# Performance work log

Measured on AMD Instinct MI355X. Metric: run time of the kernel, lower is better.

Reference implementation:

```python
import jax, jax.numpy as jnp
import numpy as np

N_LAYERS = 6
N_HEADS = 16
HIDDEN = 1024
HEAD = HIDDEN // N_HEADS  # 64
FFWD = 4096
VOCAB = 32000
WIN = 512
EMBED = 128
BATCH = 4
NEG_INF = -1.0e9


def layer_norm(x, bias, scale, eps=1e-6):
    m = jnp.mean(x, axis=-1, keepdims=True)
    v = jnp.mean(jnp.square(x - m), axis=-1, keepdims=True)
    return (x - m) * jax.lax.rsqrt(v + eps) * scale + bias


def setup_inputs() -> dict:
    key = jax.random.key(0)
    ks = jax.random.split(key, 16)

    def rn(k, shape):
        return 0.1 * jax.random.normal(k, shape, jnp.float32)

    return {
        "x_input": jax.random.randint(ks[0], (BATCH, WIN), 0, VOCAB),
        "prev_inputs": jax.random.normal(ks[1], (N_LAYERS, BATCH, WIN, HIDDEN), jnp.float32),
        "W_emb_dec": rn(ks[2], (VOCAB, EMBED)),
        "W_dec_lin": rn(ks[3], (EMBED, HIDDEN)),
        "p_decoder": rn(ks[4], (HIDDEN, VOCAB)),
        "p_d_q": rn(ks[5], (N_LAYERS, HIDDEN, HIDDEN)),
        "p_d_k": rn(ks[6], (N_LAYERS, HIDDEN, HIDDEN)),
        "p_d_v": rn(ks[7], (N_LAYERS, HIDDEN, HIDDEN)),
        "p_d_c": rn(ks[8], (N_LAYERS, HIDDEN, HIDDEN)),
        "p_d_ff1": rn(ks[9], (N_LAYERS, HIDDEN, FFWD)),
        "p_d_ff2": rn(ks[10], (N_LAYERS, FFWD, HIDDEN)),
        "b_d_ff1": jnp.zeros((N_LAYERS, FFWD), jnp.float32),
        "b_d_ff2": jnp.zeros((N_LAYERS, HIDDEN), jnp.float32),
        "b_d_bias_1": jnp.zeros((N_LAYERS, HIDDEN), jnp.float32),
        "b_d_bias_2": jnp.zeros((N_LAYERS, HIDDEN), jnp.float32),
        "b_d_scale_1": jnp.ones((N_LAYERS, HIDDEN), jnp.float32),
        "b_d_scale_2": jnp.ones((N_LAYERS, HIDDEN), jnp.float32),
        "x_emb_pos_dec": rn(ks[11], (N_LAYERS, 2 * WIN, HIDDEN)),
    }


def reference(x_input, prev_inputs, W_emb_dec, W_dec_lin, p_decoder,
              p_d_q, p_d_k, p_d_v, p_d_c, p_d_ff1, p_d_ff2,
              b_d_ff1, b_d_ff2, b_d_bias_1, b_d_bias_2,
              b_d_scale_1, b_d_scale_2, x_emb_pos_dec):
    L = x_input.shape[1]
    # token embedding (scaled by 1/sqrt(hidden)) then linear to hidden
    tok = W_emb_dec[x_input] * (HIDDEN ** -0.5)        # [B, L, E]
    h0 = jnp.einsum('ble,eh->blh', tok, W_dec_lin)     # [B, L, H]

    mask_len = L + WIN
    mask = NEG_INF * (1.0 - jnp.tril(jnp.ones((mask_len, mask_len), jnp.float32)))

    def split_heads(x):
        b, t, _ = x.shape
        return x.reshape(b, t, N_HEADS, HEAD).transpose(0, 2, 1, 3)  # [B, nH, T, d]

    def layer_fn(layer_input, p):
        Wq, Wk, Wv, Wc, Wf1, Wf2, bf1, bf2, b1, s1, b2, s2, pos, prev = p
        # concat cached window with current input, add positional embedding
        x = pos[None] + jnp.concatenate([prev, layer_input], axis=1)  # [B, 2W, H]
        q = split_heads(x @ Wq) * (HEAD ** -0.5)
        k = split_heads(x @ Wk)
        v = split_heads(x @ Wv)
        scores = jnp.einsum('bhqd,bhkd->bhqk', q, k) + mask
        alphas = jax.nn.softmax(scores, axis=-1)
        o = jnp.einsum('bhqk,bhkd->bhqd', alphas, v)
        o = o.transpose(0, 2, 1, 3).reshape(x.shape)  # combine heads
        attn = o @ Wc
        # var_type == 'norm_add': residual + LN(sublayer)
        x_self = x + layer_norm(attn, b1, s1)
        ff = jnp.maximum(x_self @ Wf1 + bf1, 0.0) @ Wf2 + bf2
        y = x_self + layer_norm(ff, b2, s2)
        new = y[:, WIN:, :]  # drop the cached-window positions
        return new, new

    params = (p_d_q, p_d_k, p_d_v, p_d_c, p_d_ff1, p_d_ff2,
              b_d_ff1, b_d_ff2, b_d_bias_1, b_d_scale_1,
              b_d_bias_2, b_d_scale_2, x_emb_pos_dec, prev_inputs)
    _, dec_outputs = jax.lax.scan(layer_fn, h0, params)  # [n_layers, B, L, H]
    dec_logits = jnp.einsum('blh,hv->blv', dec_outputs[-1], p_decoder)
    return (dec_logits, dec_outputs)
```

## Files before the change

### kernel.cpp

```cpp
#include <hip/hip_runtime.h>
#include <hip/hip_bf16.h>

#define NL   6
#define NH   16
#define HID  1024
#define HD   64
#define FFW  4096
#define VOC  32000
#define WINN 512
#define EMB  128
#define NB   4
#define TT   1024

typedef __attribute__((ext_vector_type(8))) _Float16 f16x8;
typedef __attribute__((ext_vector_type(8))) short    b16x8;
typedef __attribute__((ext_vector_type(4))) float    f32x4;

__device__ __forceinline__ ushort f2b(float f) {
    __hip_bfloat16 h = __float2bfloat16(f);
    return *reinterpret_cast<ushort*>(&h);
}
__device__ __forceinline__ void split16(float f, ushort& hb, ushort& lb) {
    _Float16 h = (_Float16)f;
    _Float16 l = (_Float16)((f - (float)h) * 2048.0f);
    hb = __builtin_bit_cast(ushort, h);
    lb = __builtin_bit_cast(ushort, l);
}
__device__ __forceinline__ void gload16(const void* g, void* l) {
    __builtin_amdgcn_global_load_lds(
        (const __attribute__((address_space(1))) unsigned int*)g,
        (__attribute__((address_space(3))) unsigned int*)l, 16, 0, 0);
}

__global__ __launch_bounds__(256) void embed_kernel(
    const int* __restrict__ xin, const float* __restrict__ Wemb,
    const float* __restrict__ Wlin, float* __restrict__ h0)
{
    int row = blockIdx.x;
    int tok = xin[row];
    __shared__ float tk[EMB];
    if (threadIdx.x < EMB) tk[threadIdx.x] = Wemb[tok * EMB + threadIdx.x] * 0.03125f;
    __syncthreads();
    for (int j = 0; j < 4; ++j) {
        int c = threadIdx.x + 256 * j;
        float acc = 0.f;
        for (int e = 0; e < EMB; ++e) acc += tk[e] * Wlin[e * HID + c];
        h0[(long)row * HID + c] = acc;
    }
}

__global__ __launch_bounds__(256) void build_x_kernel(
    const float* __restrict__ pos, const float* __restrict__ prev,
    const float* __restrict__ cur, float* __restrict__ x,
    ushort* __restrict__ xh, ushort* __restrict__ xl)
{
    int i4 = blockIdx.x * blockDim.x + threadIdx.x;
    if (i4 >= NB * TT * HID / 4) return;
    int h4 = i4 % (HID / 4);
    int bt = i4 / (HID / 4);
    int t = bt % TT, b = bt / TT;
    float4 p = ((const float4*)pos)[t * (HID / 4) + h4];
    float4 s;
    if (t < WINN) s = ((const float4*)prev)[(long)(b * WINN + t) * (HID / 4) + h4];
    else          s = ((const float4*)cur)[(long)(b * WINN + (t - WINN)) * (HID / 4) + h4];
    float4 r; r.x = p.x + s.x; r.y = p.y + s.y; r.z = p.z + s.z; r.w = p.w + s.w;
    ((float4*)x)[i4] = r;
    ushort4 uh, ul;
    split16(r.x, uh.x, ul.x); split16(r.y, uh.y, ul.y);
    split16(r.z, uh.z, ul.z); split16(r.w, uh.w, ul.w);
    ((ushort4*)xh)[i4] = uh;
    ((ushort4*)xl)[i4] = ul;
}

__global__ __launch_bounds__(256) void wsplit_kernel(
    const float* __restrict__ W, ushort* __restrict__ Wth, ushort* __restrict__ Wtl,
    int K, int N)
{
    __shared__ float ts[32][33];
    int n0 = blockIdx.x * 32, k0 = blockIdx.y * 32;
    int tr = threadIdx.x >> 5, tc = threadIdx.x & 31;
#pragma unroll
    for (int j = 0; j < 4; ++j)
        ts[tr + j * 8][tc] = W[(long)(k0 + tr + j * 8) * N + n0 + tc];
    __syncthreads();
#pragma unroll
    for (int j = 0; j < 4; ++j) {
        int n = tr + j * 8;
        ushort hb, lb;
        split16(ts[tc][n], hb, lb);
        long idx = (long)(n0 + n) * K + k0 + tc;
        Wth[idx] = hb;
        Wtl[idx] = lb;
    }
}

__global__ __launch_bounds__(256) void vtrans_kernel(
    const ushort* __restrict__ vh, const ushort* __restrict__ vl,
    ushort* __restrict__ vth, ushort* __restrict__ vtl, int src_stride)
{
    __shared__ ushort th[32][33], tl[32][33];
    int n0 = blockIdx.x * 32, r0 = blockIdx.y * 32;
    int tr = threadIdx.x >> 5, tc = threadIdx.x & 31;
#pragma unroll
    for (int j = 0; j < 4; ++j) {
        long g = (long)(r0 + tr + j * 8) * src_stride + n0 + tc;
        th[tr + j * 8][tc] = vh[g];
        tl[tr + j * 8][tc] = vl[g];
    }
    __syncthreads();
#pragma unroll
    for (int j = 0; j < 4; ++j) {
        long g = (long)(n0 + tr + j * 8) * (NB * TT) + r0 + tc;
        vth[g] = th[tc][tr + j * 8];
        vtl[g] = tl[tc][tr + j * 8];
    }
}

__global__ __launch_bounds__(256) void hgemm(
    const ushort* __restrict__ Ah, const ushort* __restrict__ Al,
    const ushort* __restrict__ Bh, const ushort* __restrict__ Bl,
    float* __restrict__ Cf0, float* __restrict__ Cf1,
    int M, int N, int K_stride, int Ksub,
    float scale, const float* __restrict__ bias, int relu, int amap)
{
    __shared__ __align__(16) ushort Ash[128 * 32];
    __shared__ __align__(16) ushort Asl[128 * 32];
    __shared__ __align__(16) ushort Bsh[64 * 32];
    __shared__ __align__(16) ushort Bsl[64 * 32];
    const int tid  = threadIdx.x;
    const int rb   = blockIdx.y * 128;
    const int cb   = blockIdx.x * 64;
    const int z    = blockIdx.z;
    const int k_off = z * Ksub;
    float* __restrict__ Cf = z ? Cf1 : Cf0;
    const float* bias_eff = (z == 0) ? bias : nullptr;
    const int wave = tid >> 6, lane = tid & 63;
    const int wr   = (wave >> 1) * 64;
    const int wc   = (wave & 1) * 32;
    const int lr   = lane & 15;
    const int kh   = lane >> 4;

    const int lrow = lane >> 2;
    const int lkc  = (lane & 3) * 8;
    int ga0 = rb + wave * 32 + lrow;
    int ga1 = ga0 + 16;
    long ma0 = amap ? (long)((ga0 >> 9) * 1024 + 512 + (ga0 & 511)) : (long)ga0;
    long ma1 = amap ? (long)((ga1 >> 9) * 1024 + 512 + (ga1 & 511)) : (long)ga1;
    const ushort* gAh0 = Ah + ma0 * K_stride + k_off + lkc;
    const ushort* gAh1 = Ah + ma1 * K_stride + k_off + lkc;
    const ushort* gAl0 = Al + ma0 * K_stride + k_off + lkc;
    const ushort* gAl1 = Al + ma1 * K_stride + k_off + lkc;
    const ushort* gBh0 = Bh + (long)(cb + wave * 16 + lrow) * K_stride + k_off + lkc;
    const ushort* gBl0 = Bl + (long)(cb + wave * 16 + lrow) * K_stride + k_off + lkc;
    ushort* lAh0 = Ash + wave * 1024;
    ushort* lAh1 = Ash + wave * 1024 + 512;
    ushort* lAl0 = Asl + wave * 1024;
    ushort* lAl1 = Asl + wave * 1024 + 512;
    ushort* lBh0 = Bsh + wave * 512;
    ushort* lBl0 = Bsl + wave * 512;

    int aoff[4], boff[2];
#pragma unroll
    for (int m = 0; m < 4; ++m) aoff[m] = (wr + m * 16 + lr) * 32 + kh * 8;
#pragma unroll
    for (int n = 0; n < 2; ++n) boff[n] = (wc + n * 16 + lr) * 32 + kh * 8;

    f32x4 accH[4][2], accL[4][2];
#pragma unroll
    for (int m = 0; m < 4; ++m)
#pragma unroll
        for (int n = 0; n < 2; ++n) {
            accH[m][n] = (f32x4){0.f, 0.f, 0.f, 0.f};
            accL[m][n] = (f32x4){0.f, 0.f, 0.f, 0.f};
        }

    for (int k0 = 0; k0 < Ksub; k0 += 32) {
        __syncthreads();
        gload16(gAh0 + k0, lAh0);
        gload16(gAh1 + k0, lAh1);
        gload16(gAl0 + k0, lAl0);
        gload16(gAl1 + k0, lAl1);
        gload16(gBh0 + k0, lBh0);
        gload16(gBl0 + k0, lBl0);
        __syncthreads();
        f16x8 afh[4], afl[4], bfh[2], bfl[2];
#pragma unroll
        for (int m = 0; m < 4; ++m) {
            afh[m] = *(const f16x8*)(Ash + aoff[m]);
            afl[m] = *(const f16x8*)(Asl + aoff[m]);
        }
#pragma unroll
        for (int n = 0; n < 2; ++n) {
            bfh[n] = *(const f16x8*)(Bsh + boff[n]);
            bfl[n] = *(const f16x8*)(Bsl + boff[n]);
        }
#pragma unroll
        for (int m = 0; m < 4; ++m)
#pragma unroll
            for (int n = 0; n < 2; ++n) {
                accH[m][n] = __builtin_amdgcn_mfma_f32_16x16x32_f16(afh[m], bfh[n], accH[m][n], 0, 0, 0);
                accL[m][n] = __builtin_amdgcn_mfma_f32_16x16x32_f16(afh[m], bfl[n], accL[m][n], 0, 0, 0);
                accL[m][n] = __builtin_amdgcn_mfma_f32_16x16x32_f16(afl[m], bfh[n], accL[m][n], 0, 0, 0);
            }
    }

#pragma unroll
    for (int m = 0; m < 4; ++m) {
        int row0 = rb + wr + m * 16 + kh * 4;
#pragma unroll
        for (int n = 0; n < 2; ++n) {
            int col = cb + wc + n * 16 + lr;
            float bv = bias_eff ? bias_eff[col] : 0.f;
#pragma unroll
            for (int r = 0; r < 4; ++r) {
                float v = (accH[m][n][r] + accL[m][n][r] * (1.f / 2048.f)) * scale + bv;
                if (relu) v = fmaxf(v, 0.f);
                Cf[(long)(row0 + r) * N + col] = v;
            }
        }
    }
}

__global__ __launch_bounds__(512) void hgemm8(
    const ushort* __restrict__ Ah, const ushort* __restrict__ Al,
    const ushort* __restrict__ Bh, const ushort* __restrict__ Bl,
    ushort* __restrict__ Chh, ushort* __restrict__ Cll,
    int M, int N, int K_stride,
    float scale, const float* __restrict__ bias, int relu)
{
    __shared__ __align__(16) ushort Ash[128 * 32];
    __shared__ __align__(16) ushort Asl[128 * 32];
    __shared__ __align__(16) ushort Bsh[128 * 32];
    __shared__ __align__(16) ushort Bsl[128 * 32];
    const int tid  = threadIdx.x;
    const int rb   = blockIdx.y * 128;
    const int cb   = blockIdx.x * 128;
    const int wave = tid >> 6, lane = tid & 63;
    const int wr   = (wave >> 2) * 64;
    const int wc   = (wave & 3) * 32;
    const int lr   = lane & 15;
    const int kh   = lane >> 4;

    const int lrow = lane >> 2;
    const int lkc  = (lane & 3) * 8;
    const ushort* gA_h = Ah + (long)(rb + wave * 16 + lrow) * K_stride + lkc;
    const ushort* gA_l = Al + (long)(rb + wave * 16 + lrow) * K_stride + lkc;
    const ushort* gB_h = Bh + (long)(cb + wave * 16 + lrow) * K_stride + lkc;
    const ushort* gB_l = Bl + (long)(cb + wave * 16 + lrow) * K_stride + lkc;
    ushort* lA_h = Ash + wave * 512;
    ushort* lA_l = Asl + wave * 512;
    ushort* lB_h = Bsh + wave * 512;
    ushort* lB_l = Bsl + wave * 512;

    int aoff[4], boff[2];
#pragma unroll
    for (int m = 0; m < 4; ++m) aoff[m] = (wr + m * 16 + lr) * 32 + kh * 8;
#pragma unroll
    for (int n = 0; n < 2; ++n) boff[n] = (wc + n * 16 + lr) * 32 + kh * 8;

    f32x4 accH[4][2], accL[4][2];
#pragma unroll
    for (int m = 0; m < 4; ++m)
#pragma unroll
        for (int n = 0; n < 2; ++n) {
            accH[m][n] = (f32x4){0.f, 0.f, 0.f, 0.f};
            accL[m][n] = (f32x4){0.f, 0.f, 0.f, 0.f};
        }

    for (int k0 = 0; k0 < K_stride; k0 += 32) {
        __syncthreads();
        gload16(gA_h + k0, lA_h);
        gload16(gA_l + k0, lA_l);
        gload16(gB_h + k0, lB_h);
        gload16(gB_l + k0, lB_l);
        __syncthreads();
        f16x8 afh[4], afl[4], bfh[2], bfl[2];
#pragma unroll
        for (int m = 0; m < 4; ++m) {
            afh[m] = *(const f16x8*)(Ash + aoff[m]);
            afl[m] = *(const f16x8*)(Asl + aoff[m]);
        }
#pragma unroll
        for (int n = 0; n < 2; ++n) {
            bfh[n] = *(const f16x8*)(Bsh + boff[n]);
            bfl[n] = *(const f16x8*)(Bsl + boff[n]);
        }
#pragma unroll
        for (int m = 0; m < 4; ++m)
#pragma unroll
            for (int n = 0; n < 2; ++n) {
                accH[m][n] = __builtin_amdgcn_mfma_f32_16x16x32_f16(afh[m], bfh[n], accH[m][n], 0, 0, 0);
                accL[m][n] = __builtin_amdgcn_mfma_f32_16x16x32_f16(afh[m], bfl[n], accL[m][n], 0, 0, 0);
                accL[m][n] = __builtin_amdgcn_mfma_f32_16x16x32_f16(afl[m], bfh[n], accL[m][n], 0, 0, 0);
            }
    }

#pragma unroll
    for (int m = 0; m < 4; ++m) {
        int row0 = rb + wr + m * 16 + kh * 4;
#pragma unroll
        for (int n = 0; n < 2; ++n) {
            int col = cb + wc + n * 16 + lr;
            float bv = bias ? bias[col] : 0.f;
#pragma unroll
            for (int r = 0; r < 4; ++r) {
                float v = (accH[m][n][r] + accL[m][n][r] * (1.f / 2048.f)) * scale + bv;
                if (relu) v = fmaxf(v, 0.f);
                long idx = (long)(row0 + r) * N + col;
                ushort hb, lb; split16(v, hb, lb);
                Chh[idx] = hb; Cll[idx] = lb;
            }
        }
    }
}

__global__ __launch_bounds__(256) void fattn_mfma(
    const float* __restrict__ qa, const float* __restrict__ qb,
    const ushort* __restrict__ kbh, const ushort* __restrict__ kbl, int kstr,
    const ushort* __restrict__ vth, const ushort* __restrict__ vtl,
    ushort* __restrict__ oh, ushort* __restrict__ ol)
{
    __shared__ __align__(16) ushort ksh[64 * 72];
    __shared__ __align__(16) ushort ksl[64 * 72];
    __shared__ __align__(16) ushort vsh[64 * 72];
    __shared__ __align__(16) ushort vsl[64 * 72];
    const int qt = blockIdx.x, h = blockIdx.y, b = blockIdx.z;
    const int tid = threadIdx.x;
    const int wave = tid >> 6, lane = tid & 63;
    const int lr = lane & 15, kg4 = lane >> 4;
    const int qbase = b * WINN + qt * 64;

    f16x8 qfh[2], qfl[2];
#pragma unroll
    for (int c = 0; c < 2; ++c) {
        long ga = (long)(qbase + wave * 16 + lr) * HID + h * HD + c * 32 + kg4 * 8;
        float4 a0 = *(const float4*)(qa + ga);
        float4 a1 = *(const float4*)(qa + ga + 4);
        float4 b0 = *(const float4*)(qb + ga);
        float4 b1 = *(const float4*)(qb + ga + 4);
        float qv[8] = {a0.x + b0.x, a0.y + b0.y, a0.z + b0.z, a0.w + b0.w,
                       a1.x + b1.x, a1.y + b1.y, a1.z + b1.z, a1.w + b1.w};
        ushort uh[8], ul[8];
#pragma unroll
        for (int j = 0; j < 8; ++j) split16(qv[j], uh[j], ul[j]);
        qfh[c] = *(const f16x8*)uh;
        qfl[c] = *(const f16x8*)ul;
    }

    f32x4 accOH[4], accOL[4];
#pragma unroll
    for (int d = 0; d < 4; ++d) {
        accOH[d] = (f32x4){0.f, 0.f, 0.f, 0.f};
        accOL[d] = (f32x4){0.f, 0.f, 0.f, 0.f};
    }
    float mrow[4], lrow[4];
#pragma unroll
    for (int r = 0; r < 4; ++r) { mrow[r] = -3.0e38f; lrow[r] = 0.f; }

    const int sr = tid >> 2;
    const int sd = (tid & 3) * 16;

    const int ktmax = 9 + qt;
    for (int kt = 0; kt < ktmax; ++kt) {
        __syncthreads();
        {
            long gk = (long)(b * TT + kt * 64 + sr) * kstr + h * HD + sd;
            uint4 h0 = *(const uint4*)(kbh + gk);
            uint4 h1 = *(const uint4*)(kbh + gk + 8);
            uint4 l0 = *(const uint4*)(kbl + gk);
            uint4 l1 = *(const uint4*)(kbl + gk + 8);
            long gv = (long)(h * HD + sr) * (NB * TT) + b * TT + kt * 64 + sd;
            uint4 vh0 = *(const uint4*)(vth + gv);
            uint4 vh1 = *(const uint4*)(vth + gv + 8);
            uint4 vl0 = *(const uint4*)(vtl + gv);
            uint4 vl1 = *(const uint4*)(vtl + gv + 8);
            *(uint4*)(ksh + sr * 72 + sd) = h0;
            *(uint4*)(ksh + sr * 72 + sd + 8) = h1;
            *(uint4*)(ksl + sr * 72 + sd) = l0;
            *(uint4*)(ksl + sr * 72 + sd + 8) = l1;
            *(uint4*)(vsh + sr * 72 + sd) = vh0;
            *(uint4*)(vsh + sr * 72 + sd + 8) = vh1;
            *(uint4*)(vsl + sr * 72 + sd) = vl0;
            *(uint4*)(vsl + sr * 72 + sd + 8) = vl1;
        }
        __syncthreads();

        f32x4 sH[4], sL[4];
#pragma unroll
        for (int n = 0; n < 4; ++n) {
            sH[n] = (f32x4){0.f, 0.f, 0.f, 0.f};
            sL[n] = (f32x4){0.f, 0.f, 0.f, 0.f};
        }
#pragma unroll
        for (int c = 0; c < 2; ++c) {
#pragma unroll
            for (int n = 0; n < 4; ++n) {
                int ad = (n * 16 + lr) * 72 + c * 32 + kg4 * 8;
                f16x8 bh = *(const f16x8*)(ksh + ad);
                f16x8 bl = *(const f16x8*)(ksl + ad);
                sH[n] = __builtin_amdgcn_mfma_f32_16x16x32_f16(qfh[c], bh, sH[n], 0, 0, 0);
                sL[n] = __builtin_amdgcn_mfma_f32_16x16x32_f16(qfh[c], bl, sL[n], 0, 0, 0);
                sL[n] = __builtin_amdgcn_mfma_f32_16x16x32_f16(qfl[c], bh, sL[n], 0, 0, 0);
            }
        }
        float S[4][4];
#pragma unroll
        for (int n = 0; n < 4; ++n)
#pragma unroll
            for (int r = 0; r < 4; ++r)
                S[n][r] = sH[n][r] + sL[n][r] * (1.f / 2048.f);

        if (kt == ktmax - 1) {
#pragma unroll
            for (int r = 0; r < 4; ++r) {
                int qi = WINN + qt * 64 + wave * 16 + kg4 * 4 + r;
#pragma unroll
                for (int n = 0; n < 4; ++n) {
                    int kg = kt * 64 + n * 16 + lr;
                    if (kg > qi) S[n][r] = -1e9f;
                }
            }
        }

#pragma unroll
        for (int r = 0; r < 4; ++r) {
            float mx = fmaxf(fmaxf(S[0][r], S[1][r]), fmaxf(S[2][r], S[3][r]));
            mx = fmaxf(mx, __shfl_xor(mx, 1));
            mx = fmaxf(mx, __shfl_xor(mx, 2));
            mx = fmaxf(mx, __shfl_xor(mx, 4));
            mx = fmaxf(mx, __shfl_xor(mx, 8));
            float mnew = fmaxf(mrow[r], mx);
            float alpha = __expf(mrow[r] - mnew);
            float rs = 0.f;
#pragma unroll
            for (int n = 0; n < 4; ++n) { S[n][r] = __expf(S[n][r] - mnew); rs += S[n][r]; }
            rs += __shfl_xor(rs, 1);
            rs += __shfl_xor(rs, 2);
            rs += __shfl_xor(rs, 4);
            rs += __shfl_xor(rs, 8);
            lrow[r] = lrow[r] * alpha + rs;
            mrow[r] = mnew;
#pragma unroll
            for (int d = 0; d < 4; ++d) { accOH[d][r] *= alpha; accOL[d][r] *= alpha; }
        }

        __syncthreads();
#pragma unroll
        for (int n = 0; n < 4; ++n)
#pragma unroll
            for (int r = 0; r < 4; ++r) {
                ushort hb, lb;
                split16(S[n][r], hb, lb);
                int ad = (wave * 16 + kg4 * 4 + r) * 72 + n * 16 + lr;
                ksh[ad] = hb;
                ksl[ad] = lb;
            }
        f16x8 pfh[2], pfl[2];
#pragma unroll
        for (int c = 0; c < 2; ++c) {
            int ad = (wave * 16 + lr) * 72 + c * 32 + kg4 * 8;
            pfh[c] = *(const f16x8*)(ksh + ad);
            pfl[c] = *(const f16x8*)(ksl + ad);
        }
#pragma unroll
        for (int c = 0; c < 2; ++c) {
#pragma unroll
            for (int d = 0; d < 4; ++d) {
                int ad = (d * 16 + lr) * 72 + c * 32 + kg4 * 8;
                f16x8 vh = *(const f16x8*)(vsh + ad);
                f16x8 vl = *(const f16x8*)(vsl + ad);
                accOH[d] = __builtin_amdgcn_mfma_f32_16x16x32_f16(pfh[c], vh, accOH[d], 0, 0, 0);
                accOL[d] = __builtin_amdgcn_mfma_f32_16x16x32_f16(pfh[c], vl, accOL[d], 0, 0, 0);
                accOL[d] = __builtin_amdgcn_mfma_f32_16x16x32_f16(pfl[c], vh, accOL[d], 0, 0, 0);
            }
        }
    }

#pragma unroll
    for (int r = 0; r < 4; ++r) {
        float inv = 1.f / lrow[r];
        long rowb = (long)(qbase + wave * 16 + kg4 * 4 + r) * HID + h * HD + lr;
#pragma unroll
        for (int d = 0; d < 4; ++d) {
            float v = (accOH[d][r] + accOL[d][r] * (1.f / 2048.f)) * inv;
            ushort hb, lb;
            split16(v, hb, lb);
            oh[rowb + d * 16] = hb;
            ol[rowb + d * 16] = lb;
        }
    }
}

__global__ __launch_bounds__(256) void transp_kernel(
    const float* __restrict__ W, ushort* __restrict__ Wt, int K, int N)
{
    __shared__ float ts[32][33];
    int n0 = blockIdx.x * 32, k0 = blockIdx.y * 32;
    int tr = threadIdx.x >> 5, tc = threadIdx.x & 31;
#pragma unroll
    for (int j = 0; j < 4; ++j)
        ts[tr + j * 8][tc] = W[(long)(k0 + tr + j * 8) * N + n0 + tc];
    __syncthreads();
#pragma unroll
    for (int j = 0; j < 4; ++j) {
        int n = tr + j * 8;
        Wt[(long)(n0 + n) * K + k0 + tc] = f2b(ts[tc][n]);
    }
}

__global__ __launch_bounds__(256) void mfma_gemm(
    const ushort* __restrict__ A, const ushort* __restrict__ Bt,
    float* __restrict__ Cf, int M, int N, int K)
{
    __shared__ __align__(16) ushort As[128 * 32];
    __shared__ __align__(16) ushort Bs[128 * 32];
    const int tid  = threadIdx.x;
    const int ntm  = M >> 7;
    const int nbx  = gridDim.x;
    const int nwg  = nbx * gridDim.y;
    const int bid  = blockIdx.y * nbx + blockIdx.x;
    const int cpx  = nwg >> 3;
    const int swz  = (bid & 7) * cpx + (bid >> 3);
    const int rb   = (swz % ntm) * 128;
    const int cb   = (swz / ntm) * 128;
    const int wave = tid >> 6, lane = tid & 63;
    const int wr   = (wave >> 1) * 64;
    const int wc   = (wave & 1) * 64;
    const int lr   = lane & 15;
    const int kh   = lane >> 4;

    const int lrow = lane >> 2;
    const int lkc  = (lane & 3) * 8;
    const ushort* gA0 = A + (long)(rb + wave * 32 + lrow) * K + lkc;
    const ushort* gA1 = A + (long)(rb + wave * 32 + 16 + lrow) * K + lkc;
    const ushort* gB0 = Bt + (long)(cb + wave * 32 + lrow) * K + lkc;
    const ushort* gB1 = Bt + (long)(cb + wave * 32 + 16 + lrow) * K + lkc;
    ushort* lA0 = As + wave * 1024;
    ushort* lA1 = As + wave * 1024 + 512;
    ushort* lB0 = Bs + wave * 1024;
    ushort* lB1 = Bs + wave * 1024 + 512;

    int aoff[4], boff[4];
#pragma unroll
    for (int m = 0; m < 4; ++m) aoff[m] = (wr + m * 16 + lr) * 32 + kh * 8;
#pragma unroll
    for (int n = 0; n < 4; ++n) boff[n] = (wc + n * 16 + lr) * 32 + kh * 8;

    f32x4 acc[4][4];
#pragma unroll
    for (int m = 0; m < 4; ++m)
#pragma unroll
        for (int n = 0; n < 4; ++n)
            acc[m][n] = (f32x4){0.f, 0.f, 0.f, 0.f};

    for (int k0 = 0; k0 < K; k0 += 32) {
        __syncthreads();
        gload16(gA0 + k0, lA0);
        gload16(gA1 + k0, lA1);
        gload16(gB0 + k0, lB0);
        gload16(gB1 + k0, lB1);
        __syncthreads();
        b16x8 af[4], bfr[4];
#pragma unroll
        for (int m = 0; m < 4; ++m) af[m] = *(const b16x8*)(As + aoff[m]);
#pragma unroll
        for (int n = 0; n < 4; ++n) bfr[n] = *(const b16x8*)(Bs + boff[n]);
#pragma unroll
        for (int m = 0; m < 4; ++m)
#pragma unroll
            for (int n = 0; n < 4; ++n)
                acc[m][n] = __builtin_amdgcn_mfma_f32_16x16x32_bf16(af[m], bfr[n], acc[m][n], 0, 0, 0);
    }

#pragma unroll
    for (int m = 0; m < 4; ++m) {
        int row0 = rb + wr + m * 16 + kh * 4;
#pragma unroll
        for (int n = 0; n < 4; ++n) {
            int col = cb + wc + n * 16 + lr;
#pragma unroll
            for (int r = 0; r < 4; ++r)
                Cf[(long)(row0 + r) * N + col] = acc[m][n][r];
        }
    }
}

__global__ __launch_bounds__(256) void ln_res_kernel(
    const float* __restrict__ t, const float* __restrict__ t2,
    const float* __restrict__ res, float* __restrict__ out,
    ushort* __restrict__ outh, ushort* __restrict__ outl, ushort* __restrict__ outb,
    const float* __restrict__ bias, const float* __restrict__ scale, int res_map)
{
    int r = blockIdx.x;
    int tid = threadIdx.x;
    long rr = res_map ? (long)((r >> 9) * 1024 + 512 + (r & 511)) : (long)r;
    float4 v = ((const float4*)(t + (long)r * HID))[tid];
    if (t2) {
        float4 w = ((const float4*)(t2 + (long)r * HID))[tid];
        v.x += w.x; v.y += w.y; v.z += w.z; v.w += w.w;
    }
    __shared__ float red[4];
    float s = v.x + v.y + v.z + v.w;
    for (int off = 32; off > 0; off >>= 1) s += __shfl_xor(s, off);
    if ((tid & 63) == 0) red[tid >> 6] = s;
    __syncthreads();
    float mean = (red[0] + red[1] + red[2] + red[3]) * (1.f / HID);
    __syncthreads();
    float dx = v.x - mean, dy = v.y - mean, dz = v.z - mean, dw = v.w - mean;
    float qs = dx * dx + dy * dy + dz * dz + dw * dw;
    for (int off = 32; off > 0; off >>= 1) qs += __shfl_xor(qs, off);
    if ((tid & 63) == 0) red[tid >> 6] = qs;
    __syncthreads();
    float var = (red[0] + red[1] + red[2] + red[3]) * (1.f / HID);
    float rs = rsqrtf(var + 1e-6f);
    float4 rv = ((const float4*)(res + rr * HID))[tid];
    float4 sc4 = ((const float4*)scale)[tid];
    float4 b4  = ((const float4*)bias)[tid];
    float4 o4;
    o4.x = rv.x + dx * rs * sc4.x + b4.x;
    o4.y = rv.y + dy * rs * sc4.y + b4.y;
    o4.z = rv.z + dz * rs * sc4.z + b4.z;
    o4.w = rv.w + dw * rs * sc4.w + b4.w;
    ((float4*)(out + (long)r * HID))[tid] = o4;
    if (outh) {
        ushort4 uh, ul;
        split16(o4.x, uh.x, ul.x); split16(o4.y, uh.y, ul.y);
        split16(o4.z, uh.z, ul.z); split16(o4.w, uh.w, ul.w);
        ((ushort4*)(outh + (long)r * HID))[tid] = uh;
        ((ushort4*)(outl + (long)r * HID))[tid] = ul;
    }
    if (outb) {
        ushort4 u; u.x = f2b(o4.x); u.y = f2b(o4.y); u.z = f2b(o4.z); u.w = f2b(o4.w);
        ((ushort4*)(outb + (long)r * HID))[tid] = u;
    }
}

extern "C" void kernel_launch(void* const* d_in, const int* in_sizes, int n_in,
                              void* d_out, int out_size, void* d_ws, size_t ws_size,
                              hipStream_t stream)
{
    const int*   x_input = (const int*)  d_in[0];
    const float* prev    = (const float*)d_in[1];
    const float* Wemb    = (const float*)d_in[2];
    const float* Wlin    = (const float*)d_in[3];
    const float* pdec    = (const float*)d_in[4];
    const float* pq      = (const float*)d_in[5];
    const float* pk      = (const float*)d_in[6];
    const float* pv      = (const float*)d_in[7];
    const float* pc      = (const float*)d_in[8];
    const float* pf1     = (const float*)d_in[9];
    const float* pf2     = (const float*)d_in[10];
    const float* bf1     = (const float*)d_in[11];
    const float* bf2     = (const float*)d_in[12];
    const float* b1      = (const float*)d_in[13];
    const float* b2      = (const float*)d_in[14];
    const float* s1      = (const float*)d_in[15];
    const float* s2      = (const float*)d_in[16];
    const float* pos     = (const float*)d_in[17];

    float* outp   = (float*)d_out;
    float* logits = outp;
    float* dec    = outp + (long)2048 * VOC;

    char* base = (char*)d_ws;
    float*  x_f   = (float*) (base + 0);
    ushort* x_hi  = (ushort*)(base + 16777216);
    ushort* x_lo  = (ushort*)(base + 25165824);
    ushort* kv_hi = (ushort*)(base + 33554432);
    ushort* kv_lo = (ushort*)(base + 50331648);
    ushort* vt_hi = (ushort*)(base + 67108864);
    ushort* vt_lo = (ushort*)(base + 75497472);
    ushort* o_hi  = (ushort*)(base + 83886080);
    ushort* o_lo  = (ushort*)(base + 88080384);
    float*  t0a   = (float*) (base + 92274688);
    float*  h0    = t0a;
    float*  qa    = t0a;
    float*  t0b   = (float*) (base + 100663296);
    float*  qb    = t0b;
    float*  xs    = (float*) (base + 109051904);
    ushort* xs_hi = (ushort*)(base + 117440512);
    ushort* xs_lo = (ushort*)(base + 121634816);
    ushort* wq_hi = (ushort*)(base + 125829120);
    ushort* wq_lo = (ushort*)(base + 127926272);
    ushort* wkv_hi= (ushort*)(base + 130023424);
    ushort* wkv_lo= (ushort*)(base + 134217728);
    ushort* wc_hi = (ushort*)(base + 138412032);
    ushort* wc_lo = (ushort*)(base + 140509184);
    ushort* wf1_hi= (ushort*)(base + 142606336);
    ushort* wf1_lo= (ushort*)(base + 150994944);
    ushort* wf2_hi= (ushort*)(base + 159383552);
    ushort* wf2_lo= (ushort*)(base + 167772160);
    ushort* ff1_hi= (ushort*)(base + 33554432);
    ushort* ff1_lo= (ushort*)(base + 50331648);
    ushort* decb  = (ushort*)(base + 83886080);
    ushort* wdect = (ushort*)(base + 0);

    embed_kernel<<<NB * WINN, 256, 0, stream>>>(x_input, Wemb, Wlin, h0);

    for (int l = 0; l < NL; ++l) {
        const float* cur = (l == 0) ? h0 : (dec + (long)(l - 1) * 2097152);
        build_x_kernel<<<(NB * TT * HID / 4) / 256, 256, 0, stream>>>(
            pos + (long)l * TT * HID, prev + (long)l * NB * WINN * HID, cur,
            x_f, x_hi, x_lo);

        wsplit_kernel<<<dim3(32, 32), 256, 0, stream>>>(pq + (long)l * HID * HID, wq_hi, wq_lo, HID, HID);
        wsplit_kernel<<<dim3(32, 32), 256, 0, stream>>>(pk + (long)l * HID * HID, wkv_hi, wkv_lo, HID, HID);
        wsplit_kernel<<<dim3(32, 32), 256, 0, stream>>>(pv + (long)l * HID * HID,
                                                        wkv_hi + (size_t)1024 * 1024,
                                                        wkv_lo + (size_t)1024 * 1024, HID, HID);
        wsplit_kernel<<<dim3(32, 32), 256, 0, stream>>>(pc + (long)l * HID * HID, wc_hi, wc_lo, HID, HID);
        wsplit_kernel<<<dim3(FFW / 32, HID / 32), 256, 0, stream>>>(
            pf1 + (long)l * HID * FFW, wf1_hi, wf1_lo, HID, FFW);
        wsplit_kernel<<<dim3(HID / 32, FFW / 32), 256, 0, stream>>>(
            pf2 + (long)l * FFW * HID, wf2_hi, wf2_lo, FFW, HID);

        hgemm8<<<dim3(2048 / 128, (NB * TT) / 128), 512, 0, stream>>>(
            x_hi, x_lo, wkv_hi, wkv_lo, kv_hi, kv_lo,
            NB * TT, 2048, HID, 1.f, nullptr, 0);
        hgemm<<<dim3(HID / 64, (NB * WINN) / 128, 2), 256, 0, stream>>>(
            x_hi, x_lo, wq_hi, wq_lo, qa, qb,
            NB * WINN, HID, HID, 512, 0.125f, nullptr, 0, 1);
        vtrans_kernel<<<dim3(HID / 32, (NB * TT) / 32), 256, 0, stream>>>(
            kv_hi + 1024, kv_lo + 1024, vt_hi, vt_lo, 2048);

        fattn_mfma<<<dim3(WINN / 64, NH, NB), 256, 0, stream>>>(
            qa, qb, kv_hi, kv_lo, 2048, vt_hi, vt_lo, o_hi, o_lo);

        hgemm<<<dim3(HID / 64, (NB * WINN) / 128, 2), 256, 0, stream>>>(
            o_hi, o_lo, wc_hi, wc_lo, t0a, t0b,
            NB * WINN, HID, HID, 512, 1.f, nullptr, 0, 0);
        ln_res_kernel<<<NB * WINN, 256, 0, stream>>>(
            t0a, t0b, x_f, xs, xs_hi, xs_lo, nullptr,
            b1 + l * HID, s1 + l * HID, 1);

        hgemm8<<<dim3(FFW / 128, (NB * WINN) / 128), 512, 0, stream>>>(
            xs_hi, xs_lo, wf1_hi, wf1_lo, ff1_hi, ff1_lo,
            NB * WINN, FFW, HID, 1.f, bf1 + l * FFW, 1);
        hgemm<<<dim3(HID / 64, (NB * WINN) / 128, 2), 256, 0, stream>>>(
            ff1_hi, ff1_lo, wf2_hi, wf2_lo, t0a, t0b,
            NB * WINN, HID, FFW, 2048, 1.f, bf2 + l * HID, 0, 0);
        ln_res_kernel<<<NB * WINN, 256, 0, stream>>>(
            t0a, t0b, xs, dec + (long)l * 2097152, nullptr, nullptr,
            (l == NL - 1) ? decb : nullptr, b2 + l * HID, s2 + l * HID, 0);
    }

    transp_kernel<<<dim3(VOC / 32, HID / 32), 256, 0, stream>>>(pdec, wdect, HID, VOC);
    mfma_gemm<<<dim3(VOC / 128, (NB * WINN) / 128), 256, 0, stream>>>(
        decb, wdect, logits, NB * WINN, VOC, HID);
}
```

Measured before the change: 2.548 ms.

## Unify GEMMs on 128x128 hgemm8, batch weight splits, prefetch K/V in attention

Removes the 128x64 hgemm kernel. The Q, output-projection and FF2 GEMMs now run through the 512-thread 128x128 hgemm8, which gains split-K, row mapping and an optional fp32 output path. The four per-layer 1024x1024 weight-split launches are merged into one launch with a z dimension. The flash attention kernel now loads the next K/V tile into registers while computing the current one, hiding global latency at the cost of more registers. The larger tile halves the block count for the N=1024 GEMMs (from 512 to 256 per launch), which may reduce occupancy.

```diff
diff --git a/kernel.cpp b/kernel.cpp
--- a/kernel.cpp
+++ b/kernel.cpp
@@ -94,6 +94,38 @@
     }
 }
 
+__global__ __launch_bounds__(256) void wsplit4_kernel(
+    const float* __restrict__ pq, const float* __restrict__ pk,
+    const float* __restrict__ pv, const float* __restrict__ pc,
+    ushort* __restrict__ wq_h, ushort* __restrict__ wq_l,
+    ushort* __restrict__ wkv_h, ushort* __restrict__ wkv_l,
+    ushort* __restrict__ wc_h, ushort* __restrict__ wc_l)
+{
+    const float* src; ushort* dh; ushort* dl;
+    switch (blockIdx.z) {
+        case 0:  src = pq; dh = wq_h;            dl = wq_l;            break;
+        case 1:  src = pk; dh = wkv_h;           dl = wkv_l;           break;
+        case 2:  src = pv; dh = wkv_h + 1048576; dl = wkv_l + 1048576; break;
+        default: src = pc; dh = wc_h;            dl = wc_l;            break;
+    }
+    __shared__ float ts[32][33];
+    int n0 = blockIdx.x * 32, k0 = blockIdx.y * 32;
+    int tr = threadIdx.x >> 5, tc = threadIdx.x & 31;
+#pragma unroll
+    for (int j = 0; j < 4; ++j)
+        ts[tr + j * 8][tc] = src[(long)(k0 + tr + j * 8) * HID + n0 + tc];
+    __syncthreads();
+#pragma unroll
+    for (int j = 0; j < 4; ++j) {
+        int n = tr + j * 8;
+        ushort hb, lb;
+        split16(ts[tc][n], hb, lb);
+        long idx = (long)(n0 + n) * HID + k0 + tc;
+        dh[idx] = hb;
+        dl[idx] = lb;
+    }
+}
+
 __global__ __launch_bounds__(256) void vtrans_kernel(
     const ushort* __restrict__ vh, const ushort* __restrict__ vl,
     ushort* __restrict__ vth, ushort* __restrict__ vtl, int src_stride)
@@ -116,117 +148,13 @@
     }
 }
 
-__global__ __launch_bounds__(256) void hgemm(
-    const ushort* __restrict__ Ah, const ushort* __restrict__ Al,
-    const ushort* __restrict__ Bh, const ushort* __restrict__ Bl,
-    float* __restrict__ Cf0, float* __restrict__ Cf1,
-    int M, int N, int K_stride, int Ksub,
-    float scale, const float* __restrict__ bias, int relu, int amap)
-{
-    __shared__ __align__(16) ushort Ash[128 * 32];
-    __shared__ __align__(16) ushort Asl[128 * 32];
-    __shared__ __align__(16) ushort Bsh[64 * 32];
-    __shared__ __align__(16) ushort Bsl[64 * 32];
-    const int tid  = threadIdx.x;
-    const int rb   = blockIdx.y * 128;
-    const int cb   = blockIdx.x * 64;
-    const int z    = blockIdx.z;
-    const int k_off = z * Ksub;
-    float* __restrict__ Cf = z ? Cf1 : Cf0;
-    const float* bias_eff = (z == 0) ? bias : nullptr;
-    const int wave = tid >> 6, lane = tid & 63;
-    const int wr   = (wave >> 1) * 64;
-    const int wc   = (wave & 1) * 32;
-    const int lr   = lane & 15;
-    const int kh   = lane >> 4;
-
-    const int lrow = lane >> 2;
-    const int lkc  = (lane & 3) * 8;
-    int ga0 = rb + wave * 32 + lrow;
-    int ga1 = ga0 + 16;
-    long ma0 = amap ? (long)((ga0 >> 9) * 1024 + 512 + (ga0 & 511)) : (long)ga0;
-    long ma1 = amap ? (long)((ga1 >> 9) * 1024 + 512 + (ga1 & 511)) : (long)ga1;
-    const ushort* gAh0 = Ah + ma0 * K_stride + k_off + lkc;
-    const ushort* gAh1 = Ah + ma1 * K_stride + k_off + lkc;
-    const ushort* gAl0 = Al + ma0 * K_stride + k_off + lkc;
-    const ushort* gAl1 = Al + ma1 * K_stride + k_off + lkc;
-    const ushort* gBh0 = Bh + (long)(cb + wave * 16 + lrow) * K_stride + k_off + lkc;
-    const ushort* gBl0 = Bl + (long)(cb + wave * 16 + lrow) * K_stride + k_off + lkc;
-    ushort* lAh0 = Ash + wave * 1024;
-    ushort* lAh1 = Ash + wave * 1024 + 512;
-    ushort* lAl0 = Asl + wave * 1024;
-    ushort* lAl1 = Asl + wave * 1024 + 512;
-    ushort* lBh0 = Bsh + wave * 512;
-    ushort* lBl0 = Bsl + wave * 512;
-
-    int aoff[4], boff[2];
-#pragma unroll
-    for (int m = 0; m < 4; ++m) aoff[m] = (wr + m * 16 + lr) * 32 + kh * 8;
-#pragma unroll
-    for (int n = 0; n < 2; ++n) boff[n] = (wc + n * 16 + lr) * 32 + kh * 8;
-
-    f32x4 accH[4][2], accL[4][2];
-#pragma unroll
-    for (int m = 0; m < 4; ++m)
-#pragma unroll
-        for (int n = 0; n < 2; ++n) {
-            accH[m][n] = (f32x4){0.f, 0.f, 0.f, 0.f};
-            accL[m][n] = (f32x4){0.f, 0.f, 0.f, 0.f};
-        }
-
-    for (int k0 = 0; k0 < Ksub; k0 += 32) {
-        __syncthreads();
-        gload16(gAh0 + k0, lAh0);
-        gload16(gAh1 + k0, lAh1);
-        gload16(gAl0 + k0, lAl0);
-        gload16(gAl1 + k0, lAl1);
-        gload16(gBh0 + k0, lBh0);
-        gload16(gBl0 + k0, lBl0);
-        __syncthreads();
-        f16x8 afh[4], afl[4], bfh[2], bfl[2];
-#pragma unroll
-        for (int m = 0; m < 4; ++m) {
-            afh[m] = *(const f16x8*)(Ash + aoff[m]);
-            afl[m] = *(const f16x8*)(Asl + aoff[m]);
-        }
-#pragma unroll
-        for (int n = 0; n < 2; ++n) {
-            bfh[n] = *(const f16x8*)(Bsh + boff[n]);
-            bfl[n] = *(const f16x8*)(Bsl + boff[n]);
-        }
-#pragma unroll
-        for (int m = 0; m < 4; ++m)
-#pragma unroll
-            for (int n = 0; n < 2; ++n) {
-                accH[m][n] = __builtin_amdgcn_mfma_f32_16x16x32_f16(afh[m], bfh[n], accH[m][n], 0, 0, 0);
-                accL[m][n] = __builtin_amdgcn_mfma_f32_16x16x32_f16(afh[m], bfl[n], accL[m][n], 0, 0, 0);
-                accL[m][n] = __builtin_amdgcn_mfma_f32_16x16x32_f16(afl[m], bfh[n], accL[m][n], 0, 0, 0);
-            }
-    }
-
-#pragma unroll
-    for (int m = 0; m < 4; ++m) {
-        int row0 = rb + wr + m * 16 + kh * 4;
-#pragma unroll
-        for (int n = 0; n < 2; ++n) {
-            int col = cb + wc + n * 16 + lr;
-            float bv = bias_eff ? bias_eff[col] : 0.f;
-#pragma unroll
-            for (int r = 0; r < 4; ++r) {
-                float v = (accH[m][n][r] + accL[m][n][r] * (1.f / 2048.f)) * scale + bv;
-                if (relu) v = fmaxf(v, 0.f);
-                Cf[(long)(row0 + r) * N + col] = v;
-            }
-        }
-    }
-}
-
 __global__ __launch_bounds__(512) void hgemm8(
     const ushort* __restrict__ Ah, const ushort* __restrict__ Al,
     const ushort* __restrict__ Bh, const ushort* __restrict__ Bl,
     ushort* __restrict__ Chh, ushort* __restrict__ Cll,
-    int M, int N, int K_stride,
-    float scale, const float* __restrict__ bias, int relu)
+    float* __restrict__ Cf0, float* __restrict__ Cf1,
+    int M, int N, int K_stride, int Ksub,
+    float scale, const float* __restrict__ bias, int relu, int amap)
 {
     __shared__ __align__(16) ushort Ash[128 * 32];
     __shared__ __align__(16) ushort Asl[128 * 32];
@@ -235,6 +163,8 @@
     const int tid  = threadIdx.x;
     const int rb   = blockIdx.y * 128;
     const int cb   = blockIdx.x * 128;
+    const int z    = blockIdx.z;
+    const int k_off = z * Ksub;
     const int wave = tid >> 6, lane = tid & 63;
     const int wr   = (wave >> 2) * 64;
     const int wc   = (wave & 3) * 32;
@@ -243,10 +173,12 @@
 
     const int lrow = lane >> 2;
     const int lkc  = (lane & 3) * 8;
-    const ushort* gA_h = Ah + (long)(rb + wave * 16 + lrow) * K_stride + lkc;
-    const ushort* gA_l = Al + (long)(rb + wave * 16 + lrow) * K_stride + lkc;
-    const ushort* gB_h = Bh + (long)(cb + wave * 16 + lrow) * K_stride + lkc;
-    const ushort* gB_l = Bl + (long)(cb + wave * 16 + lrow) * K_stride + lkc;
+    int gra = rb + wave * 16 + lrow;
+    long marow = amap ? (long)((gra >> 9) * 1024 + 512 + (gra & 511)) : (long)gra;
+    const ushort* gA_h = Ah + marow * K_stride + k_off + lkc;
+    const ushort* gA_l = Al + marow * K_stride + k_off + lkc;
+    const ushort* gB_h = Bh + (long)(cb + wave * 16 + lrow) * K_stride + k_off + lkc;
+    const ushort* gB_l = Bl + (long)(cb + wave * 16 + lrow) * K_stride + k_off + lkc;
     ushort* lA_h = Ash + wave * 512;
     ushort* lA_l = Asl + wave * 512;
     ushort* lB_h = Bsh + wave * 512;
@@ -267,7 +199,7 @@
             accL[m][n] = (f32x4){0.f, 0.f, 0.f, 0.f};
         }
 
-    for (int k0 = 0; k0 < K_stride; k0 += 32) {
+    for (int k0 = 0; k0 < Ksub; k0 += 32) {
         __syncthreads();
         gload16(gA_h + k0, lA_h);
         gload16(gA_l + k0, lA_l);
@@ -295,20 +227,40 @@
             }
     }
 
-#pragma unroll
-    for (int m = 0; m < 4; ++m) {
-        int row0 = rb + wr + m * 16 + kh * 4;
-#pragma unroll
-        for (int n = 0; n < 2; ++n) {
-            int col = cb + wc + n * 16 + lr;
-            float bv = bias ? bias[col] : 0.f;
-#pragma unroll
-            for (int r = 0; r < 4; ++r) {
-                float v = (accH[m][n][r] + accL[m][n][r] * (1.f / 2048.f)) * scale + bv;
-                if (relu) v = fmaxf(v, 0.f);
-                long idx = (long)(row0 + r) * N + col;
-                ushort hb, lb; split16(v, hb, lb);
-                Chh[idx] = hb; Cll[idx] = lb;
+    if (Cf0) {
+        float* __restrict__ Cf = z ? Cf1 : Cf0;
+        const float* bias_eff = (z == 0) ? bias : nullptr;
+#pragma unroll
+        for (int m = 0; m < 4; ++m) {
+            int row0 = rb + wr + m * 16 + kh * 4;
+#pragma unroll
+            for (int n = 0; n < 2; ++n) {
+                int col = cb + wc + n * 16 + lr;
+                float bv = bias_eff ? bias_eff[col] : 0.f;
+#pragma unroll
+                for (int r = 0; r < 4; ++r) {
+                    float v = (accH[m][n][r] + accL[m][n][r] * (1.f / 2048.f)) * scale + bv;
+                    if (relu) v = fmaxf(v, 0.f);
+                    Cf[(long)(row0 + r) * N + col] = v;
+                }
+            }
+        }
+    } else {
+#pragma unroll
+        for (int m = 0; m < 4; ++m) {
+            int row0 = rb + wr + m * 16 + kh * 4;
+#pragma unroll
+            for (int n = 0; n < 2; ++n) {
+                int col = cb + wc + n * 16 + lr;
+                float bv = bias ? bias[col] : 0.f;
+#pragma unroll
+                for (int r = 0; r < 4; ++r) {
+                    float v = (accH[m][n][r] + accL[m][n][r] * (1.f / 2048.f)) * scale + bv;
+                    if (relu) v = fmaxf(v, 0.f);
+                    long idx = (long)(row0 + r) * N + col;
+                    ushort hb, lb; split16(v, hb, lb);
+                    Chh[idx] = hb; Cll[idx] = lb;
+                }
             }
         }
     }
@@ -360,29 +312,27 @@
     const int sr = tid >> 2;
     const int sd = (tid & 3) * 16;
 
+    uint4 rk0, rk1, rk2, rk3, rv0, rv1, rv2, rv3;
+    {
+        long gk = (long)(b * TT + sr) * kstr + h * HD + sd;
+        rk0 = *(const uint4*)(kbh + gk); rk1 = *(const uint4*)(kbh + gk + 8);
+        rk2 = *(const uint4*)(kbl + gk); rk3 = *(const uint4*)(kbl + gk + 8);
+        long gv = (long)(h * HD + sr) * (NB * TT) + b * TT + sd;
+        rv0 = *(const uint4*)(vth + gv); rv1 = *(const uint4*)(vth + gv + 8);
+        rv2 = *(const uint4*)(vtl + gv); rv3 = *(const uint4*)(vtl + gv + 8);
+    }
+
     const int ktmax = 9 + qt;
     for (int kt = 0; kt < ktmax; ++kt) {
         __syncthreads();
-        {
-            long gk = (long)(b * TT + kt * 64 + sr) * kstr + h * HD + sd;
-            uint4 h0 = *(const uint4*)(kbh + gk);
-            uint4 h1 = *(const uint4*)(kbh + gk + 8);
-            uint4 l0 = *(const uint4*)(kbl + gk);
-            uint4 l1 = *(const uint4*)(kbl + gk + 8);
-            long gv = (long)(h * HD + sr) * (NB * TT) + b * TT + kt * 64 + sd;
-            uint4 vh0 = *(const uint4*)(vth + gv);
-            uint4 vh1 = *(const uint4*)(vth + gv + 8);
-            uint4 vl0 = *(const uint4*)(vtl + gv);
-            uint4 vl1 = *(const uint4*)(vtl + gv + 8);
-            *(uint4*)(ksh + sr * 72 + sd) = h0;
-            *(uint4*)(ksh + sr * 72 + sd + 8) = h1;
-            *(uint4*)(ksl + sr * 72 + sd) = l0;
-            *(uint4*)(ksl + sr * 72 + sd + 8) = l1;
-            *(uint4*)(vsh + sr * 72 + sd) = vh0;
-            *(uint4*)(vsh + sr * 72 + sd + 8) = vh1;
-            *(uint4*)(vsl + sr * 72 + sd) = vl0;
-            *(uint4*)(vsl + sr * 72 + sd + 8) = vl1;
-        }
+        *(uint4*)(ksh + sr * 72 + sd) = rk0;
+        *(uint4*)(ksh + sr * 72 + sd + 8) = rk1;
+        *(uint4*)(ksl + sr * 72 + sd) = rk2;
+        *(uint4*)(ksl + sr * 72 + sd + 8) = rk3;
+        *(uint4*)(vsh + sr * 72 + sd) = rv0;
+        *(uint4*)(vsh + sr * 72 + sd + 8) = rv1;
+        *(uint4*)(vsl + sr * 72 + sd) = rv2;
+        *(uint4*)(vsl + sr * 72 + sd + 8) = rv3;
         __syncthreads();
 
         f32x4 sH[4], sL[4];
@@ -403,6 +353,16 @@
                 sL[n] = __builtin_amdgcn_mfma_f32_16x16x32_f16(qfl[c], bh, sL[n], 0, 0, 0);
             }
         }
+
+        if (kt + 1 < ktmax) {
+            long gk = (long)(b * TT + (kt + 1) * 64 + sr) * kstr + h * HD + sd;
+            rk0 = *(const uint4*)(kbh + gk); rk1 = *(const uint4*)(kbh + gk + 8);
+            rk2 = *(const uint4*)(kbl + gk); rk3 = *(const uint4*)(kbl + gk + 8);
+            long gv = (long)(h * HD + sr) * (NB * TT) + b * TT + (kt + 1) * 64 + sd;
+            rv0 = *(const uint4*)(vth + gv); rv1 = *(const uint4*)(vth + gv + 8);
+            rv2 = *(const uint4*)(vtl + gv); rv3 = *(const uint4*)(vtl + gv + 8);
+        }
+
         float S[4][4];
 #pragma unroll
         for (int n = 0; n < 4; ++n)
@@ -703,22 +663,20 @@
             pos + (long)l * TT * HID, prev + (long)l * NB * WINN * HID, cur,
             x_f, x_hi, x_lo);
 
-        wsplit_kernel<<<dim3(32, 32), 256, 0, stream>>>(pq + (long)l * HID * HID, wq_hi, wq_lo, HID, HID);
-        wsplit_kernel<<<dim3(32, 32), 256, 0, stream>>>(pk + (long)l * HID * HID, wkv_hi, wkv_lo, HID, HID);
-        wsplit_kernel<<<dim3(32, 32), 256, 0, stream>>>(pv + (long)l * HID * HID,
-                                                        wkv_hi + (size_t)1024 * 1024,
-                                                        wkv_lo + (size_t)1024 * 1024, HID, HID);
-        wsplit_kernel<<<dim3(32, 32), 256, 0, stream>>>(pc + (long)l * HID * HID, wc_hi, wc_lo, HID, HID);
+        wsplit4_kernel<<<dim3(32, 32, 4), 256, 0, stream>>>(
+            pq + (long)l * HID * HID, pk + (long)l * HID * HID,
+            pv + (long)l * HID * HID, pc + (long)l * HID * HID,
+            wq_hi, wq_lo, wkv_hi, wkv_lo, wc_hi, wc_lo);
         wsplit_kernel<<<dim3(FFW / 32, HID / 32), 256, 0, stream>>>(
             pf1 + (long)l * HID * FFW, wf1_hi, wf1_lo, HID, FFW);
         wsplit_kernel<<<dim3(HID / 32, FFW / 32), 256, 0, stream>>>(
             pf2 + (long)l * FFW * HID, wf2_hi, wf2_lo, FFW, HID);
 
-        hgemm8<<<dim3(2048 / 128, (NB * TT) / 128), 512, 0, stream>>>(
-            x_hi, x_lo, wkv_hi, wkv_lo, kv_hi, kv_lo,
-            NB * TT, 2048, HID, 1.f, nullptr, 0);
-        hgemm<<<dim3(HID / 64, (NB * WINN) / 128, 2), 256, 0, stream>>>(
-            x_hi, x_lo, wq_hi, wq_lo, qa, qb,
+        hgemm8<<<dim3(2048 / 128, (NB * TT) / 128, 1), 512, 0, stream>>>(
+            x_hi, x_lo, wkv_hi, wkv_lo, kv_hi, kv_lo, nullptr, nullptr,
+            NB * TT, 2048, HID, HID, 1.f, nullptr, 0, 0);
+        hgemm8<<<dim3(HID / 128, (NB * WINN) / 128, 2), 512, 0, stream>>>(
+            x_hi, x_lo, wq_hi, wq_lo, nullptr, nullptr, qa, qb,
             NB * WINN, HID, HID, 512, 0.125f, nullptr, 0, 1);
         vtrans_kernel<<<dim3(HID / 32, (NB * TT) / 32), 256, 0, stream>>>(
             kv_hi + 1024, kv_lo + 1024, vt_hi, vt_lo, 2048);
@@ -726,18 +684,18 @@
         fattn_mfma<<<dim3(WINN / 64, NH, NB), 256, 0, stream>>>(
             qa, qb, kv_hi, kv_lo, 2048, vt_hi, vt_lo, o_hi, o_lo);
 
-        hgemm<<<dim3(HID / 64, (NB * WINN) / 128, 2), 256, 0, stream>>>(
-            o_hi, o_lo, wc_hi, wc_lo, t0a, t0b,
+        hgemm8<<<dim3(HID / 128, (NB * WINN) / 128, 2), 512, 0, stream>>>(
+            o_hi, o_lo, wc_hi, wc_lo, nullptr, nullptr, t0a, t0b,
             NB * WINN, HID, HID, 512, 1.f, nullptr, 0, 0);
         ln_res_kernel<<<NB * WINN, 256, 0, stream>>>(
             t0a, t0b, x_f, xs, xs_hi, xs_lo, nullptr,
             b1 + l * HID, s1 + l * HID, 1);
 
-        hgemm8<<<dim3(FFW / 128, (NB * WINN) / 128), 512, 0, stream>>>(
-            xs_hi, xs_lo, wf1_hi, wf1_lo, ff1_hi, ff1_lo,
-            NB * WINN, FFW, HID, 1.f, bf1 + l * FFW, 1);
-        hgemm<<<dim3(HID / 64, (NB * WINN) / 128, 2), 256, 0, stream>>>(
-            ff1_hi, ff1_lo, wf2_hi, wf2_lo, t0a, t0b,
+        hgemm8<<<dim3(FFW / 128, (NB * WINN) / 128, 1), 512, 0, stream>>>(
+            xs_hi, xs_lo, wf1_hi, wf1_lo, ff1_hi, ff1_lo, nullptr, nullptr,
+            NB * WINN, FFW, HID, HID, 1.f, bf1 + l * FFW, 1, 0);
+        hgemm8<<<dim3(HID / 128, (NB * WINN) / 128, 2), 512, 0, stream>>>(
+            ff1_hi, ff1_lo, wf2_hi, wf2_lo, nullptr, nullptr, t0a, t0b,
             NB * WINN, HID, FFW, 2048, 1.f, bf2 + l * HID, 0, 0);
         ln_res_kernel<<<NB * WINN, 256, 0, stream>>>(
             t0a, t0b, xs, dec + (long)l * 2097152, nullptr, nullptr,
```

Result: no change. 2.528 ms (-0.8%).
